# Optimization experiments

Measured on AMD Instinct MI355X. Metric: run time of the kernel, lower is better.

Reference implementation:

```python
import jax, jax.numpy as jnp
import numpy as np

ALPHA = 0.1
K = 5


def setup_inputs() -> dict:
    key = jax.random.key(0)
    ks = jax.random.split(key, 6)
    N, E = 50000, 800000
    IN, HID, OUT = 512, 256, 64
    x = jax.random.normal(ks[0], (N, IN), dtype=jnp.float32)
    edge_index = jax.random.randint(ks[1], (2, E), 0, N, dtype=jnp.int64)
    # Linear params (torch Linear: y = x @ W.T + b), kaiming-ish scale
    W1 = jax.random.normal(ks[2], (HID, IN), dtype=jnp.float32) / np.sqrt(IN)
    b1 = jnp.zeros((HID,), dtype=jnp.float32)
    W2 = jax.random.normal(ks[3], (OUT, HID), dtype=jnp.float32) / np.sqrt(HID)
    b2 = jnp.zeros((OUT,), dtype=jnp.float32)
    return {"x": x, "W1": W1, "b1": b1, "W2": W2, "b2": b2,
            "edge_index": edge_index}


def reference(x, W1, b1, W2, b2, edge_index):
    N = x.shape[0]
    # --- MLP encoder (eval mode: dropout is identity) ---
    h = jax.nn.relu(x @ W1.T + b1)          # [N, HID]
    h = h @ W2.T + b2                       # [N, OUT]

    # --- gcn_norm with self-loops (PyG APPNP default) ---
    src, dst = edge_index[0], edge_index[1]
    loop = jnp.arange(N, dtype=src.dtype)
    src_f = jnp.concatenate([src, loop])    # [E+N]
    dst_f = jnp.concatenate([dst, loop])
    ew = jnp.ones(src_f.shape[0], dtype=h.dtype)
    deg = jax.ops.segment_sum(ew, dst_f, num_segments=N)
    dinv = jnp.where(deg > 0, jax.lax.rsqrt(deg), 0.0)
    norm = dinv[src_f] * dinv[dst_f]        # [E+N]

    # --- K iterations of personalized-PageRank propagation ---
    def body(xk, _):
        msg = norm[:, None] * xk[src_f]                      # gather [E+N, OUT]
        agg = jax.ops.segment_sum(msg, dst_f, num_segments=N)
        return (1.0 - ALPHA) * agg + ALPHA * h, None

    xK, _ = jax.lax.scan(body, h, None, length=K)
    return jax.nn.log_softmax(xK, axis=1)
```

## Files before the change

kernel.cpp:

```cpp
#include <hip/hip_runtime.h>
#include <hip/hip_bf16.h>

#define IN_DIM  512
#define HID_DIM 256
#define OUT_DIM 64

typedef __attribute__((ext_vector_type(8))) short bf16x8;
typedef __attribute__((ext_vector_type(4))) float f32x4;

static __device__ __forceinline__ ushort f2b(float f) {
    __hip_bfloat16 b = __float2bfloat16(f);
    return *reinterpret_cast<ushort*>(&b);
}
static __device__ __forceinline__ float b2f_lo(uint u) {
    union { uint u; float f; } t; t.u = u << 16; return t.f;
}
static __device__ __forceinline__ float b2f_hi(uint u) {
    union { uint u; float f; } t; t.u = u & 0xFFFF0000u; return t.f;
}
static __device__ __forceinline__ uint packbf(float x, float y) {
    return (uint)f2b(x) | ((uint)f2b(y) << 16);
}

#define GLOAD16(g, l) __builtin_amdgcn_global_load_lds(                      \
    (const __attribute__((address_space(1))) void*)(g),                      \
    (__attribute__((address_space(3))) void*)(l), 16, 0, 0)


__global__ __launch_bounds__(256) void f2b_kernel(const float* __restrict__ in,
                                                  ushort* __restrict__ out, int n8) {
    for (int i = blockIdx.x * 256 + threadIdx.x; i < n8; i += gridDim.x * 256) {
        float4 a = *reinterpret_cast<const float4*>(&in[(size_t)i * 8]);
        float4 b = *reinterpret_cast<const float4*>(&in[(size_t)i * 8 + 4]);
        ushort4 lo = make_ushort4(f2b(a.x), f2b(a.y), f2b(a.z), f2b(a.w));
        ushort4 hi = make_ushort4(f2b(b.x), f2b(b.y), f2b(b.z), f2b(b.w));
        *reinterpret_cast<ushort4*>(&out[(size_t)i * 8])     = lo;
        *reinterpret_cast<ushort4*>(&out[(size_t)i * 8 + 4]) = hi;
    }
}


__global__ void hist_kernel(const int* __restrict__ ei, int* __restrict__ deg, int E) {
    int e = blockIdx.x * 256 + threadIdx.x;
    if (e < E) atomicAdd(&deg[ei[E + e]], 1);
}

__global__ __launch_bounds__(256) void scanA_kernel(const int* __restrict__ deg,
                                                    int* __restrict__ offs,
                                                    int* __restrict__ bsum, int N) {
    __shared__ int sh[256];
    int tid = threadIdx.x;
    int i = blockIdx.x * 256 + tid;
    int v = (i < N) ? deg[i] : 0;
    sh[tid] = v;
    __syncthreads();
#pragma unroll
    for (int off = 1; off < 256; off <<= 1) {
        int t = (tid >= off) ? sh[tid - off] : 0;
        __syncthreads();
        sh[tid] += t;
        __syncthreads();
    }
    if (i < N) offs[i] = sh[tid] - v;
    if (tid == 255) bsum[blockIdx.x] = sh[255];
}

__global__ __launch_bounds__(256) void scanB_kernel(int* __restrict__ bsum, int nb) {
    __shared__ int sh[256];
    int tid = threadIdx.x;
    int v = (tid < nb) ? bsum[tid] : 0;
    sh[tid] = v;
    __syncthreads();
#pragma unroll
    for (int off = 1; off < 256; off <<= 1) {
        int t = (tid >= off) ? sh[tid - off] : 0;
        __syncthreads();
        sh[tid] += t;
        __syncthreads();
    }
    if (tid < nb) bsum[tid] = sh[tid] - v;
}

__global__ __launch_bounds__(256) void scanC_kernel(const int* __restrict__ deg,
                                                    const int* __restrict__ bsum,
                                                    int* __restrict__ offs,
                                                    float* __restrict__ dinv,
                                                    int N, int E) {
    int i = blockIdx.x * 256 + threadIdx.x;
    if (i < N) {
        offs[i] += bsum[i >> 8];
        dinv[i] = rsqrtf((float)(deg[i] + 1));
    }
    if (i == 0) offs[N] = E;
}

__global__ void fill_kernel(const int* __restrict__ ei, const int* __restrict__ offs,
                            int* __restrict__ cursor, const float* __restrict__ dinv,
                            uint* __restrict__ edat, int E) {
    int e = blockIdx.x * 256 + threadIdx.x;
    if (e < E) {
        int s = ei[e];
        int d = ei[E + e];
        int pos = offs[d] + atomicAdd(&cursor[d], 1);
        edat[pos] = (uint)s | ((uint)f2b(dinv[d] * dinv[s]) << 16);
    }
}


__global__ __launch_bounds__(256) void gemm1_f32a(const float* __restrict__ A,
                                                  const ushort* __restrict__ B,
                                                  const float* __restrict__ bias,
                                                  ushort* __restrict__ C, int M) {
    constexpr int K = IN_DIM;
    constexpr int NK = K / 64;
    __shared__ float  Asf[128 * 64];
    __shared__ ushort Bs[128 * 64];

    const int tid  = threadIdx.x;
    const int lane = tid & 63;
    const int wid  = tid >> 6;
    const int wm = wid >> 1, wn = wid & 1;
    const int m0 = blockIdx.y * 128;
    const int n0 = blockIdx.x * 128;
    const int l15 = lane & 15;
    const int lq  = lane >> 4;

    const int a_r   = lane >> 4;
    const int a_s16 = lane & 15;
    const int a_pair = a_s16 >> 1, a_sub = a_s16 & 1;
    const int srow  = lane >> 3;
    const int sslot = (lane & 7) ^ srow;

    f32x4 acc[4][4];
#pragma unroll
    for (int i = 0; i < 4; ++i)
#pragma unroll
        for (int j = 0; j < 4; ++j) acc[i][j] = (f32x4)0.0f;

    for (int ks = 0; ks < NK; ++ks) {
        const int k0 = ks * 64;
#pragma unroll
        for (int q = 0; q < 4; ++q) {
            const int rbase = (wid * 4 + q) * 8;
            const int row = rbase + srow;
            const ushort* gb = B + (size_t)(n0 + row) * K + k0 + sslot * 8;
            GLOAD16(gb, &Bs[rbase * 64]);
        }
#pragma unroll
        for (int q = 0; q < 8; ++q) {
            const int rbase = (wid * 8 + q) * 4;
            const int row = rbase + a_r;
            int am = m0 + row; if (am >= M) am = M - 1;
            const int col = k0 + ((a_pair ^ (row & 7)) << 3) + (a_sub << 2);
            const float* ga = A + (size_t)am * K + col;
            GLOAD16(ga, &Asf[rbase * 64]);
        }
        __syncthreads();
#pragma unroll
        for (int kk = 0; kk < 2; ++kk) {
            const int p = kk * 4 + lq;
            bf16x8 af[4], bf[4];
#pragma unroll
            for (int f = 0; f < 4; ++f) {
                const int ar = wm * 64 + f * 16 + l15;
                const int fi = ar * 64 + ((p ^ (ar & 7)) << 3);
                f32x4 v0 = *reinterpret_cast<const f32x4*>(&Asf[fi]);
                f32x4 v1 = *reinterpret_cast<const f32x4*>(&Asf[fi + 4]);
                bf16x8 a;
                a[0] = (short)f2b(v0[0]); a[1] = (short)f2b(v0[1]);
                a[2] = (short)f2b(v0[2]); a[3] = (short)f2b(v0[3]);
                a[4] = (short)f2b(v1[0]); a[5] = (short)f2b(v1[1]);
                a[6] = (short)f2b(v1[2]); a[7] = (short)f2b(v1[3]);
                af[f] = a;
                const int br = wn * 64 + f * 16 + l15;
                bf[f] = *reinterpret_cast<const bf16x8*>(&Bs[br * 64 + ((p ^ (br & 7)) << 3)]);
            }
#pragma unroll
            for (int i = 0; i < 4; ++i)
#pragma unroll
                for (int j = 0; j < 4; ++j)
                    acc[i][j] = __builtin_amdgcn_mfma_f32_16x16x32_bf16(af[i], bf[j], acc[i][j], 0, 0, 0);
        }
        __syncthreads();
    }

    const int lr = lq * 4;
#pragma unroll
    for (int nf = 0; nf < 4; ++nf) {
        int col = n0 + wn * 64 + nf * 16 + l15;
        float bv = bias[col];
#pragma unroll
        for (int mf = 0; mf < 4; ++mf) {
#pragma unroll
            for (int j = 0; j < 4; ++j) {
                int row = m0 + wm * 64 + mf * 16 + lr + j;
                if (row < M) {
                    float v = fmaxf(acc[mf][nf][j] + bv, 0.f);
                    C[(size_t)row * HID_DIM + col] = f2b(v);
                }
            }
        }
    }
}


#define LDT 40

__global__ __launch_bounds__(256) void gemm2_bf16(const ushort* __restrict__ A,
                                                  const float* __restrict__ B,
                                                  const float* __restrict__ bias,
                                                  ushort* __restrict__ Cb,
                                                  int M) {
    constexpr int K = HID_DIM;
    constexpr int NK = K / 32;
    __shared__ ushort As[128 * LDT];
    __shared__ ushort Bs[64 * LDT];

    const int tid = threadIdx.x;
    const int lane = tid & 63;
    const int wid = tid >> 6;
    const int wm = wid >> 1, wn = wid & 1;
    const int m0 = blockIdx.x * 128;
    const int l15 = lane & 15;
    const int koff = (lane >> 4) * 8;

    f32x4 acc[4][2];
#pragma unroll
    for (int i = 0; i < 4; ++i)
#pragma unroll
        for (int j = 0; j < 2; ++j) acc[i][j] = (f32x4)0.0f;

    uint4 rawA[2];
    float4 rbv[2];
#pragma unroll
    for (int i = 0; i < 2; ++i) {
        int slot = tid + i * 256;
        int rowA = slot >> 2, c8 = (slot & 3) << 3;
        int m = m0 + rowA;
        rawA[i] = (m < M) ? *reinterpret_cast<const uint4*>(&A[(size_t)m * K + c8])
                          : make_uint4(0u, 0u, 0u, 0u);
        int rowB = slot >> 3, c4 = (slot & 7) << 2;
        rbv[i] = *reinterpret_cast<const float4*>(&B[(size_t)rowB * K + c4]);
    }
#pragma unroll
    for (int i = 0; i < 2; ++i) {
        int slot = tid + i * 256;
        int rowA = slot >> 2, c8 = (slot & 3) << 3;
        *reinterpret_cast<uint4*>(&As[rowA * LDT + c8]) = rawA[i];
        int rowB = slot >> 3, c4 = (slot & 7) << 2;
        ushort4 ub = make_ushort4(f2b(rbv[i].x), f2b(rbv[i].y), f2b(rbv[i].z), f2b(rbv[i].w));
        *reinterpret_cast<ushort4*>(&Bs[rowB * LDT + c4]) = ub;
    }
    __syncthreads();

    for (int ks = 0; ks < NK; ++ks) {
        if (ks + 1 < NK) {
            int k0 = (ks + 1) * 32;
#pragma unroll
            for (int i = 0; i < 2; ++i) {
                int slot = tid + i * 256;
                int rowA = slot >> 2, c8 = (slot & 3) << 3;
                int m = m0 + rowA;
                rawA[i] = (m < M) ? *reinterpret_cast<const uint4*>(&A[(size_t)m * K + k0 + c8])
                                  : make_uint4(0u, 0u, 0u, 0u);
                int rowB = slot >> 3, c4 = (slot & 7) << 2;
                rbv[i] = *reinterpret_cast<const float4*>(&B[(size_t)rowB * K + k0 + c4]);
            }
        }
        bf16x8 af[4], bf[2];
#pragma unroll
        for (int f = 0; f < 4; ++f)
            af[f] = *reinterpret_cast<const bf16x8*>(&As[(wm * 64 + f * 16 + l15) * LDT + koff]);
#pragma unroll
        for (int f = 0; f < 2; ++f)
            bf[f] = *reinterpret_cast<const bf16x8*>(&Bs[(wn * 32 + f * 16 + l15) * LDT + koff]);
#pragma unroll
        for (int i = 0; i < 4; ++i)
#pragma unroll
            for (int j = 0; j < 2; ++j)
                acc[i][j] = __builtin_amdgcn_mfma_f32_16x16x32_bf16(af[i], bf[j], acc[i][j], 0, 0, 0);
        __syncthreads();
        if (ks + 1 < NK) {
#pragma unroll
            for (int i = 0; i < 2; ++i) {
                int slot = tid + i * 256;
                int rowA = slot >> 2, c8 = (slot & 3) << 3;
                *reinterpret_cast<uint4*>(&As[rowA * LDT + c8]) = rawA[i];
                int rowB = slot >> 3, c4 = (slot & 7) << 2;
                ushort4 ub = make_ushort4(f2b(rbv[i].x), f2b(rbv[i].y), f2b(rbv[i].z), f2b(rbv[i].w));
                *reinterpret_cast<ushort4*>(&Bs[rowB * LDT + c4]) = ub;
            }
            __syncthreads();
        }
    }

    const int lr = (lane >> 4) * 4;
#pragma unroll
    for (int nf = 0; nf < 2; ++nf) {
        int col = wn * 32 + nf * 16 + l15;
        float bv = bias[col];
#pragma unroll
        for (int mf = 0; mf < 4; ++mf) {
#pragma unroll
            for (int j = 0; j < 4; ++j) {
                int row = m0 + wm * 64 + mf * 16 + lr + j;
                if (row < M)
                    Cb[(size_t)row * OUT_DIM + col] = f2b(acc[mf][nf][j] + bv);
            }
        }
    }
}


__global__ __launch_bounds__(256) void propb_kernel(const uint* __restrict__ xin,
                                                    const uint* __restrict__ hb,
                                                    const float* __restrict__ dinv,
                                                    const int* __restrict__ offs,
                                                    const uint* __restrict__ edat,
                                                    uint* __restrict__ xout, int N) {
    int node = blockIdx.x * 8 + (threadIdx.x >> 5);
    int l32 = threadIdx.x & 31;
    if (node >= N) return;
    int e0 = offs[node], e1 = offs[node + 1];

    float ax[4] = {0.f, 0.f, 0.f, 0.f};
    float ay[4] = {0.f, 0.f, 0.f, 0.f};
    int e = e0;
    for (; e + 8 <= e1; e += 8) {
        uint p0 = edat[e+0], p1 = edat[e+1], p2 = edat[e+2], p3 = edat[e+3];
        uint p4 = edat[e+4], p5 = edat[e+5], p6 = edat[e+6], p7 = edat[e+7];
        uint g0 = xin[(size_t)(p0 & 0xFFFFu) * 32 + l32];
        uint g1 = xin[(size_t)(p1 & 0xFFFFu) * 32 + l32];
        uint g2 = xin[(size_t)(p2 & 0xFFFFu) * 32 + l32];
        uint g3 = xin[(size_t)(p3 & 0xFFFFu) * 32 + l32];
        uint g4 = xin[(size_t)(p4 & 0xFFFFu) * 32 + l32];
        uint g5 = xin[(size_t)(p5 & 0xFFFFu) * 32 + l32];
        uint g6 = xin[(size_t)(p6 & 0xFFFFu) * 32 + l32];
        uint g7 = xin[(size_t)(p7 & 0xFFFFu) * 32 + l32];
        ax[0] = fmaf(b2f_hi(p0), b2f_lo(g0), ax[0]); ay[0] = fmaf(b2f_hi(p0), b2f_hi(g0), ay[0]);
        ax[1] = fmaf(b2f_hi(p1), b2f_lo(g1), ax[1]); ay[1] = fmaf(b2f_hi(p1), b2f_hi(g1), ay[1]);
        ax[2] = fmaf(b2f_hi(p2), b2f_lo(g2), ax[2]); ay[2] = fmaf(b2f_hi(p2), b2f_hi(g2), ay[2]);
        ax[3] = fmaf(b2f_hi(p3), b2f_lo(g3), ax[3]); ay[3] = fmaf(b2f_hi(p3), b2f_hi(g3), ay[3]);
        ax[0] = fmaf(b2f_hi(p4), b2f_lo(g4), ax[0]); ay[0] = fmaf(b2f_hi(p4), b2f_hi(g4), ay[0]);
        ax[1] = fmaf(b2f_hi(p5), b2f_lo(g5), ax[1]); ay[1] = fmaf(b2f_hi(p5), b2f_hi(g5), ay[1]);
        ax[2] = fmaf(b2f_hi(p6), b2f_lo(g6), ax[2]); ay[2] = fmaf(b2f_hi(p6), b2f_hi(g6), ay[2]);
        ax[3] = fmaf(b2f_hi(p7), b2f_lo(g7), ax[3]); ay[3] = fmaf(b2f_hi(p7), b2f_hi(g7), ay[3]);
    }
    for (; e < e1; ++e) {
        uint p = edat[e];
        uint g = xin[(size_t)(p & 0xFFFFu) * 32 + l32];
        ax[0] = fmaf(b2f_hi(p), b2f_lo(g), ax[0]);
        ay[0] = fmaf(b2f_hi(p), b2f_hi(g), ay[0]);
    }
    float sx = (ax[0] + ax[1]) + (ax[2] + ax[3]);
    float sy = (ay[0] + ay[1]) + (ay[2] + ay[3]);
    float di = dinv[node];
    uint gs = xin[(size_t)node * 32 + l32];
    sx = fmaf(di * di, b2f_lo(gs), sx);
    sy = fmaf(di * di, b2f_hi(gs), sy);
    uint ah = hb[(size_t)node * 32 + l32];
    float r0 = 0.9f * sx + 0.1f * b2f_lo(ah);
    float r1 = 0.9f * sy + 0.1f * b2f_hi(ah);
    xout[(size_t)node * 32 + l32] = packbf(r0, r1);
}


__global__ __launch_bounds__(256) void propb_lsm_kernel(const uint* __restrict__ xin,
                                                        const uint* __restrict__ hb,
                                                        const float* __restrict__ dinv,
                                                        const int* __restrict__ offs,
                                                        const uint* __restrict__ edat,
                                                        float* __restrict__ out, int N) {
    int node = blockIdx.x * 8 + (threadIdx.x >> 5);
    int l32 = threadIdx.x & 31;
    if (node >= N) return;
    int e0 = offs[node], e1 = offs[node + 1];

    float ax[4] = {0.f, 0.f, 0.f, 0.f};
    float ay[4] = {0.f, 0.f, 0.f, 0.f};
    int e = e0;
    for (; e + 8 <= e1; e += 8) {
        uint p0 = edat[e+0], p1 = edat[e+1], p2 = edat[e+2], p3 = edat[e+3];
        uint p4 = edat[e+4], p5 = edat[e+5], p6 = edat[e+6], p7 = edat[e+7];
        uint g0 = xin[(size_t)(p0 & 0xFFFFu) * 32 + l32];
        uint g1 = xin[(size_t)(p1 & 0xFFFFu) * 32 + l32];
        uint g2 = xin[(size_t)(p2 & 0xFFFFu) * 32 + l32];
        uint g3 = xin[(size_t)(p3 & 0xFFFFu) * 32 + l32];
        uint g4 = xin[(size_t)(p4 & 0xFFFFu) * 32 + l32];
        uint g5 = xin[(size_t)(p5 & 0xFFFFu) * 32 + l32];
        uint g6 = xin[(size_t)(p6 & 0xFFFFu) * 32 + l32];
        uint g7 = xin[(size_t)(p7 & 0xFFFFu) * 32 + l32];
        ax[0] = fmaf(b2f_hi(p0), b2f_lo(g0), ax[0]); ay[0] = fmaf(b2f_hi(p0), b2f_hi(g0), ay[0]);
        ax[1] = fmaf(b2f_hi(p1), b2f_lo(g1), ax[1]); ay[1] = fmaf(b2f_hi(p1), b2f_hi(g1), ay[1]);
        ax[2] = fmaf(b2f_hi(p2), b2f_lo(g2), ax[2]); ay[2] = fmaf(b2f_hi(p2), b2f_hi(g2), ay[2]);
        ax[3] = fmaf(b2f_hi(p3), b2f_lo(g3), ax[3]); ay[3] = fmaf(b2f_hi(p3), b2f_hi(g3), ay[3]);
        ax[0] = fmaf(b2f_hi(p4), b2f_lo(g4), ax[0]); ay[0] = fmaf(b2f_hi(p4), b2f_hi(g4), ay[0]);
        ax[1] = fmaf(b2f_hi(p5), b2f_lo(g5), ax[1]); ay[1] = fmaf(b2f_hi(p5), b2f_hi(g5), ay[1]);
        ax[2] = fmaf(b2f_hi(p6), b2f_lo(g6), ax[2]); ay[2] = fmaf(b2f_hi(p6), b2f_hi(g6), ay[2]);
        ax[3] = fmaf(b2f_hi(p7), b2f_lo(g7), ax[3]); ay[3] = fmaf(b2f_hi(p7), b2f_hi(g7), ay[3]);
    }
    for (; e < e1; ++e) {
        uint p = edat[e];
        uint g = xin[(size_t)(p & 0xFFFFu) * 32 + l32];
        ax[0] = fmaf(b2f_hi(p), b2f_lo(g), ax[0]);
        ay[0] = fmaf(b2f_hi(p), b2f_hi(g), ay[0]);
    }
    float sx = (ax[0] + ax[1]) + (ax[2] + ax[3]);
    float sy = (ay[0] + ay[1]) + (ay[2] + ay[3]);
    float di = dinv[node];
    uint gs = xin[(size_t)node * 32 + l32];
    sx = fmaf(di * di, b2f_lo(gs), sx);
    sy = fmaf(di * di, b2f_hi(gs), sy);
    uint ah = hb[(size_t)node * 32 + l32];
    float r0 = 0.9f * sx + 0.1f * b2f_lo(ah);
    float r1 = 0.9f * sy + 0.1f * b2f_hi(ah);

    float m = fmaxf(r0, r1);
    for (int o = 16; o > 0; o >>= 1) m = fmaxf(m, __shfl_xor(m, o));
    float sum = expf(r0 - m) + expf(r1 - m);
    for (int o = 16; o > 0; o >>= 1) sum += __shfl_xor(sum, o);
    float ls = logf(sum);
    float2 o2 = make_float2(r0 - m - ls, r1 - m - ls);
    *reinterpret_cast<float2*>(&out[(size_t)node * 64 + l32 * 2]) = o2;
}


static inline size_t align256(size_t x) { return (x + 255) & ~(size_t)255; }

extern "C" void kernel_launch(void* const* d_in, const int* in_sizes, int n_in,
                              void* d_out, int out_size, void* d_ws, size_t ws_size,
                              hipStream_t stream) {
    const float* x  = (const float*)d_in[0];
    const float* W1 = (const float*)d_in[1];
    const float* b1 = (const float*)d_in[2];
    const float* W2 = (const float*)d_in[3];
    const float* b2 = (const float*)d_in[4];
    const int*   ei = (const int*)d_in[5];

    const int N = in_sizes[0] / IN_DIM;
    const int E = in_sizes[5] / 2;
    const int nb = (N + 255) / 256;

    char* base = (char*)d_ws;
    size_t off = 0;
    uint*  hb  = (uint*)(base + off);    off += align256((size_t)N * 32 * 4);
    uint*  xsa = (uint*)(base + off);    off += align256((size_t)N * 32 * 4);
    uint*  xsb = (uint*)(base + off);    off += align256((size_t)N * 32 * 4);
    ushort* w1b = (ushort*)(base + off); off += align256((size_t)HID_DIM * IN_DIM * 2);
    ushort* h1  = (ushort*)(base + off); off += align256((size_t)N * HID_DIM * 2);
    float* dinv = (float*)(base + off);  off += align256((size_t)N * 4);
    int*   deg  = (int*)(base + off);    off += align256((size_t)N * 4);
    int*   offs = (int*)(base + off);    off += align256((size_t)(N + 1) * 4);
    int*   cur  = (int*)(base + off);    off += align256((size_t)N * 4);
    int*   bsum = (int*)(base + off);    off += align256((size_t)nb * 4);
    uint*  edat = (uint*)(base + off);   off += align256((size_t)E * 4);

    hipMemsetAsync(deg, 0, (size_t)N * 4, stream);
    hipMemsetAsync(cur, 0, (size_t)N * 4, stream);
    hist_kernel<<<(E + 255) / 256, 256, 0, stream>>>(ei, deg, E);
    scanA_kernel<<<nb, 256, 0, stream>>>(deg, offs, bsum, N);
    scanB_kernel<<<1, 256, 0, stream>>>(bsum, nb);
    scanC_kernel<<<nb, 256, 0, stream>>>(deg, bsum, offs, dinv, N, E);
    fill_kernel<<<(E + 255) / 256, 256, 0, stream>>>(ei, offs, cur, dinv, edat, E);

    f2b_kernel<<<64, 256, 0, stream>>>(W1, w1b, HID_DIM * IN_DIM / 8);

    {
        dim3 g(HID_DIM / 128, (N + 127) / 128);
        gemm1_f32a<<<g, 256, 0, stream>>>(x, w1b, b1, h1, N);
    }
    {
        dim3 g((N + 127) / 128);
        gemm2_bf16<<<g, 256, 0, stream>>>(h1, W2, b2, (ushort*)hb, N);
    }

    int blocks = (N + 7) / 8;
    propb_kernel<<<blocks, 256, 0, stream>>>(hb,  hb, dinv, offs, edat, xsa, N);
    propb_kernel<<<blocks, 256, 0, stream>>>(xsa, hb, dinv, offs, edat, xsb, N);
    propb_kernel<<<blocks, 256, 0, stream>>>(xsb, hb, dinv, offs, edat, xsa, N);
    propb_kernel<<<blocks, 256, 0, stream>>>(xsa, hb, dinv, offs, edat, xsb, N);
    propb_lsm_kernel<<<blocks, 256, 0, stream>>>(xsb, hb, dinv, offs, edat,
                                                 (float*)d_out, N);
}
```

Baseline: 281.9 us.

## Double-buffer GEMM1 LDS tiles with K-step 32 to overlap loads and MFMA

Restructures the first GEMM's main loop to use two LDS buffers of half the K-depth (32 instead of 64), so the next tile's global-to-LDS loads are issued while the current tile is consumed by MFMAs. Swizzle patterns for the A (fp32) and B (bf16) tiles are redone for the narrower rows. The aim is to hide global memory latency behind compute. In exchange there are twice as many loop iterations, and the single barrier per iteration may not fully ensure the async LDS loads have completed before they are read.

```diff
diff --git a/kernel.cpp b/kernel.cpp
--- a/kernel.cpp
+++ b/kernel.cpp
@@ -112,9 +112,9 @@
                                                   const float* __restrict__ bias,
                                                   ushort* __restrict__ C, int M) {
     constexpr int K = IN_DIM;
-    constexpr int NK = K / 64;
-    __shared__ float  Asf[128 * 64];
-    __shared__ ushort Bs[128 * 64];
+    constexpr int NK = K / 32;
+    __shared__ float  Asf[2][128 * 32];
+    __shared__ ushort Bs[2][128 * 32];
 
     const int tid  = threadIdx.x;
     const int lane = tid & 63;
@@ -125,11 +125,10 @@
     const int l15 = lane & 15;
     const int lq  = lane >> 4;
 
-    const int a_r   = lane >> 4;
-    const int a_s16 = lane & 15;
-    const int a_pair = a_s16 >> 1, a_sub = a_s16 & 1;
-    const int srow  = lane >> 3;
-    const int sslot = (lane & 7) ^ srow;
+    const int a_row  = lane >> 3;
+    const int a_slot = (lane & 7) ^ a_row;
+    const int b_row  = lane >> 2;
+    const int b_slot = (lane & 3) ^ ((lane >> 3) & 3);
 
     f32x4 acc[4][4];
 #pragma unroll
@@ -137,50 +136,54 @@
 #pragma unroll
         for (int j = 0; j < 4; ++j) acc[i][j] = (f32x4)0.0f;
 
-    for (int ks = 0; ks < NK; ++ks) {
-        const int k0 = ks * 64;
+    auto stage = [&](int buf, int ks) {
+        const int k0 = ks * 32;
 #pragma unroll
         for (int q = 0; q < 4; ++q) {
             const int rbase = (wid * 4 + q) * 8;
-            const int row = rbase + srow;
-            const ushort* gb = B + (size_t)(n0 + row) * K + k0 + sslot * 8;
-            GLOAD16(gb, &Bs[rbase * 64]);
-        }
-#pragma unroll
-        for (int q = 0; q < 8; ++q) {
-            const int rbase = (wid * 8 + q) * 4;
-            const int row = rbase + a_r;
-            int am = m0 + row; if (am >= M) am = M - 1;
-            const int col = k0 + ((a_pair ^ (row & 7)) << 3) + (a_sub << 2);
-            const float* ga = A + (size_t)am * K + col;
-            GLOAD16(ga, &Asf[rbase * 64]);
-        }
-        __syncthreads();
-#pragma unroll
-        for (int kk = 0; kk < 2; ++kk) {
-            const int p = kk * 4 + lq;
-            bf16x8 af[4], bf[4];
-#pragma unroll
-            for (int f = 0; f < 4; ++f) {
-                const int ar = wm * 64 + f * 16 + l15;
-                const int fi = ar * 64 + ((p ^ (ar & 7)) << 3);
-                f32x4 v0 = *reinterpret_cast<const f32x4*>(&Asf[fi]);
-                f32x4 v1 = *reinterpret_cast<const f32x4*>(&Asf[fi + 4]);
-                bf16x8 a;
-                a[0] = (short)f2b(v0[0]); a[1] = (short)f2b(v0[1]);
-                a[2] = (short)f2b(v0[2]); a[3] = (short)f2b(v0[3]);
-                a[4] = (short)f2b(v1[0]); a[5] = (short)f2b(v1[1]);
-                a[6] = (short)f2b(v1[2]); a[7] = (short)f2b(v1[3]);
-                af[f] = a;
-                const int br = wn * 64 + f * 16 + l15;
-                bf[f] = *reinterpret_cast<const bf16x8*>(&Bs[br * 64 + ((p ^ (br & 7)) << 3)]);
-            }
-#pragma unroll
-            for (int i = 0; i < 4; ++i)
-#pragma unroll
-                for (int j = 0; j < 4; ++j)
-                    acc[i][j] = __builtin_amdgcn_mfma_f32_16x16x32_bf16(af[i], bf[j], acc[i][j], 0, 0, 0);
-        }
+            int am = m0 + rbase + a_row; if (am >= M) am = M - 1;
+            const float* ga = A + (size_t)am * K + k0 + a_slot * 4;
+            GLOAD16(ga, &Asf[buf][rbase * 32]);
+        }
+#pragma unroll
+        for (int q = 0; q < 2; ++q) {
+            const int rbase = (wid * 2 + q) * 16;
+            const int row = rbase + b_row;
+            const ushort* gb = B + (size_t)(n0 + row) * K + k0 + b_slot * 8;
+            GLOAD16(gb, &Bs[buf][rbase * 32]);
+        }
+    };
+
+    stage(0, 0);
+    __syncthreads();
+
+#pragma unroll 2
+    for (int ks = 0; ks < NK; ++ks) {
+        const int cur = ks & 1;
+        if (ks + 1 < NK) stage(cur ^ 1, ks + 1);
+
+        bf16x8 af[4], bf[4];
+#pragma unroll
+        for (int f = 0; f < 4; ++f) {
+            const int ar = wm * 64 + f * 16 + l15;
+            const int r7 = ar & 7;
+            f32x4 v0 = *reinterpret_cast<const f32x4*>(&Asf[cur][ar * 32 + (((2 * lq) ^ r7) << 2)]);
+            f32x4 v1 = *reinterpret_cast<const f32x4*>(&Asf[cur][ar * 32 + (((2 * lq + 1) ^ r7) << 2)]);
+            bf16x8 a;
+            a[0] = (short)f2b(v0[0]); a[1] = (short)f2b(v0[1]);
+            a[2] = (short)f2b(v0[2]); a[3] = (short)f2b(v0[3]);
+            a[4] = (short)f2b(v1[0]); a[5] = (short)f2b(v1[1]);
+            a[6] = (short)f2b(v1[2]); a[7] = (short)f2b(v1[3]);
+            af[f] = a;
+            const int br = wn * 64 + f * 16 + l15;
+            bf[f] = *reinterpret_cast<const bf16x8*>(&Bs[cur][br * 32 + ((lq ^ ((br >> 1) & 3)) << 3)]);
+        }
+#pragma unroll
+        for (int i = 0; i < 4; ++i)
+#pragma unroll
+            for (int j = 0; j < 4; ++j)
+                acc[i][j] = __builtin_amdgcn_mfma_f32_16x16x32_bf16(af[i], bf[j], acc[i][j], 0, 0, 0);
+
         __syncthreads();
     }
 
```

After: 284.4 us. About the same (+0.9%).
